# Optimization experiments

Measured on AMD Instinct MI355X. Metric: run time of the kernel, lower is better.

## Reference

```python
import jax, jax.numpy as jnp
import numpy as np
import math

D_MODEL = 768
NHEAD = 12
NUM_LAYERS = 6
INPUT_DIM = 768
HEAD_DIM = D_MODEL // NHEAD
D_FF = 4 * D_MODEL
TOTAL_HEADS = NUM_LAYERS * NHEAD
B, N = 4, 512


def _ln(x, g, b, eps=1e-5):
    mu = jnp.mean(x, axis=-1, keepdims=True)
    var = jnp.mean((x - mu) ** 2, axis=-1, keepdims=True)
    return (x - mu) * jax.lax.rsqrt(var + eps) * g + b


def setup_inputs() -> dict:
    key = jax.random.key(0)
    ks = iter(jax.random.split(key, 32))
    s = 0.02  # init scale keeps sigmoid scores away from saturation
    d = {
        "sentence_embeddings": jax.random.normal(next(ks), (B, N, INPUT_DIM), jnp.float32),
        "Win": jax.random.normal(next(ks), (D_MODEL, INPUT_DIM), jnp.float32) * s,
        "b_in": jnp.zeros((D_MODEL,), jnp.float32),
        "Wq": jax.random.normal(next(ks), (NUM_LAYERS, D_MODEL, D_MODEL), jnp.float32) * s,
        "bq": jnp.zeros((NUM_LAYERS, D_MODEL), jnp.float32),
        "Wk": jax.random.normal(next(ks), (NUM_LAYERS, D_MODEL, D_MODEL), jnp.float32) * s,
        "bk": jnp.zeros((NUM_LAYERS, D_MODEL), jnp.float32),
        "Wv": jax.random.normal(next(ks), (NUM_LAYERS, D_MODEL, D_MODEL), jnp.float32) * s,
        "bv": jnp.zeros((NUM_LAYERS, D_MODEL), jnp.float32),
        "Wo": jax.random.normal(next(ks), (NUM_LAYERS, D_MODEL, D_MODEL), jnp.float32) * s,
        "bo": jnp.zeros((NUM_LAYERS, D_MODEL), jnp.float32),
        "g1": jnp.ones((NUM_LAYERS, D_MODEL), jnp.float32),
        "be1": jnp.zeros((NUM_LAYERS, D_MODEL), jnp.float32),
        "g2": jnp.ones((NUM_LAYERS, D_MODEL), jnp.float32),
        "be2": jnp.zeros((NUM_LAYERS, D_MODEL), jnp.float32),
        "W1": jax.random.normal(next(ks), (NUM_LAYERS, D_FF, D_MODEL), jnp.float32) * s,
        "bf1": jnp.zeros((NUM_LAYERS, D_FF), jnp.float32),
        "W2": jax.random.normal(next(ks), (NUM_LAYERS, D_MODEL, D_FF), jnp.float32) * s,
        "bf2": jnp.zeros((NUM_LAYERS, D_MODEL), jnp.float32),
        "Wr1": jax.random.normal(next(ks), (D_MODEL // 2, D_MODEL), jnp.float32) * s,
        "br1": jnp.zeros((D_MODEL // 2,), jnp.float32),
        "Wr2": jax.random.normal(next(ks), (TOTAL_HEADS, D_MODEL // 2), jnp.float32) * s,
        "br2": jnp.zeros((TOTAL_HEADS,), jnp.float32),
        "agg_bias": jnp.zeros((1,), jnp.float32),
    }
    return d


def _forward(sentence_embeddings, Win, b_in, Wq, bq, Wk, bk, Wv, bv, Wo, bo,
             g1, be1, g2, be2, W1, bf1, W2, bf2, Wr1, br1, Wr2, br2, agg_bias):
    b, n, _ = sentence_embeddings.shape
    x = sentence_embeddings @ Win.T + b_in  # [B,N,D]
    off_diag = (1.0 - jnp.eye(n, dtype=x.dtype))[None, None]  # [1,1,N,N]
    scale = 1.0 / math.sqrt(HEAD_DIM)
    all_scores = []
    for i in range(NUM_LAYERS):
        n1 = _ln(x, g1[i], be1[i])
        q = (n1 @ Wq[i].T + bq[i]).reshape(b, n, NHEAD, HEAD_DIM).transpose(0, 2, 1, 3)
        k = (n1 @ Wk[i].T + bk[i]).reshape(b, n, NHEAD, HEAD_DIM).transpose(0, 2, 1, 3)
        v = (n1 @ Wv[i].T + bv[i]).reshape(b, n, NHEAD, HEAD_DIM).transpose(0, 2, 1, 3)
        scores = jnp.einsum('bhnd,bhmd->bhnm', q, k) * scale
        probs = jax.nn.sigmoid(scores)  # [B,H,N,N]
        row_sums = probs.sum(axis=-1, keepdims=True) + 1e-6
        attn = jnp.einsum('bhnm,bhmd->bhnd', probs, v) / row_sums
        attn = attn.transpose(0, 2, 1, 3).reshape(b, n, D_MODEL)
        x = x + attn @ Wo[i].T + bo[i]
        n2 = _ln(x, g2[i], be2[i])
        ff = jax.nn.gelu(n2 @ W1[i].T + bf1[i], approximate=False) @ W2[i].T + bf2[i]
        x = x + ff
        all_scores.append(probs * off_diag)  # zero the diagonal
    raw_w = jax.nn.gelu(x @ Wr1.T + br1, approximate=False) @ Wr2.T + br2  # [B,N,LH]
    stacked = jnp.concatenate(all_scores, axis=1)  # [B, L*H, N, N]
    final = jnp.einsum('bnh,bhnm->bnm', raw_w, stacked)
    return final + agg_bias[0]


def reference(sentence_embeddings, Win, b_in, Wq, bq, Wk, bk, Wv, bv, Wo, bo,
              g1, be1, g2, be2, W1, bf1, W2, bf2, Wr1, br1, Wr2, br2, agg_bias):
    return _forward(sentence_embeddings, Win, b_in, Wq, bq, Wk, bk, Wv, bv, Wo, bo,
                    g1, be1, g2, be2, W1, bf1, W2, bf2, Wr1, br1, Wr2, br2, agg_bias)
```

## Files before the change

kernel.cpp:

```cpp
#include <hip/hip_runtime.h>
#include <stdint.h>

#define LAYERS 6
#define BB 4
#define NSEQ 512
#define DM 768
#define NH 12
#define HD 64
#define DFF 3072
#define MTOK 2048
#define QKVN 2304
#define DR1 384
#define TH 72

typedef __attribute__((ext_vector_type(8))) short bf16x8;
typedef __attribute__((ext_vector_type(4))) float f32x4;

__device__ __forceinline__ unsigned short f2bf(float f) {
  union { float f; uint32_t u; } v; v.f = f;
  return (unsigned short)((v.u + 0x7fffu + ((v.u >> 16) & 1u)) >> 16);
}
__device__ __forceinline__ float bf2f(unsigned short h) {
  union { uint32_t u; float f; } v; v.u = ((uint32_t)h) << 16;
  return v.f;
}
__device__ __forceinline__ void gload16(const void* g, void* l) {
  __builtin_amdgcn_global_load_lds((const __attribute__((address_space(1))) void*)g,
                                   (__attribute__((address_space(3))) void*)l, 16, 0, 0);
}
#define MFMA(a, b, c) __builtin_amdgcn_mfma_f32_16x16x32_bf16(a, b, c, 0, 0, 0)

__device__ __forceinline__ float sigmoid8(float s) {
  float e, r;
  float t = s * -0.18033688011112443f;
  asm("v_exp_f32 %0, %1" : "=v"(e) : "v"(t));
  float d = 1.0f + e;
  asm("v_rcp_f32 %0, %1" : "=v"(r) : "v"(d));
  return r;
}

__global__ void cvt_f32_bf16(const float* __restrict__ s, unsigned short* __restrict__ d, int n4) {
  int i = blockIdx.x * blockDim.x + threadIdx.x;
  if (i >= n4) return;
  float4 v = reinterpret_cast<const float4*>(s)[i];
  ushort4 o;
  o.x = f2bf(v.x); o.y = f2bf(v.y); o.z = f2bf(v.z); o.w = f2bf(v.w);
  reinterpret_cast<ushort4*>(d)[i] = o;
}

__global__ void convert_layer(const float* __restrict__ wq, const float* __restrict__ wk,
                              const float* __restrict__ wv, const float* __restrict__ wo,
                              const float* __restrict__ w1, const float* __restrict__ w2,
                              const float* __restrict__ bq, const float* __restrict__ bk,
                              const float* __restrict__ bv,
                              unsigned short* __restrict__ qkvw, float* __restrict__ qkvb,
                              unsigned short* __restrict__ wow, unsigned short* __restrict__ w1w,
                              unsigned short* __restrict__ w2w) {
  const int A4 = (QKVN * DM) / 4;
  const int B4 = (DM * DM) / 4;
  const int C4 = (DFF * DM) / 4;
  int i = blockIdx.x * blockDim.x + threadIdx.x;
  if (i < QKVN / 4) {
    int j = i * 4;
    #pragma unroll
    for (int t = 0; t < 4; ++t) {
      int jj = j + t;
      int seg = jj / DM, c = jj % DM;
      const float* src = (seg == 0) ? bq : ((seg == 1) ? bk : bv);
      qkvb[jj] = src[c];
    }
  }
  const float* s4; unsigned short* dst;
  if (i < A4) {
    int j = i * 4; int row = j / DM; int c = j % DM;
    const float* w = (row < DM) ? wq : ((row < 2 * DM) ? wk : wv);
    s4 = w + (size_t)(row % DM) * DM + c; dst = qkvw + j;
  } else if (i < A4 + B4) {
    int j = (i - A4) * 4; s4 = wo + j; dst = wow + j;
  } else if (i < A4 + B4 + C4) {
    int j = (i - A4 - B4) * 4; s4 = w1 + j; dst = w1w + j;
  } else if (i < A4 + B4 + 2 * C4) {
    int j = (i - A4 - B4 - C4) * 4; s4 = w2 + j; dst = w2w + j;
  } else return;
  float4 v = *reinterpret_cast<const float4*>(s4);
  ushort4 o;
  o.x = f2bf(v.x); o.y = f2bf(v.y); o.z = f2bf(v.z); o.w = f2bf(v.w);
  *reinterpret_cast<ushort4*>(dst) = o;
}

__global__ __launch_bounds__(256) void ln_kernel(const float* __restrict__ x,
                                                 const float* __restrict__ g,
                                                 const float* __restrict__ b,
                                                 unsigned short* __restrict__ out) {
  int wave = threadIdx.x >> 6;
  int lane = threadIdx.x & 63;
  int row = blockIdx.x * 4 + wave;
  const float* xr = x + (size_t)row * DM;
  float v[12];
  #pragma unroll
  for (int c = 0; c < 3; ++c) {
    float4 t = *reinterpret_cast<const float4*>(xr + lane * 12 + c * 4);
    v[c * 4 + 0] = t.x; v[c * 4 + 1] = t.y; v[c * 4 + 2] = t.z; v[c * 4 + 3] = t.w;
  }
  float s = 0.f, s2 = 0.f;
  #pragma unroll
  for (int c = 0; c < 12; ++c) { s += v[c]; s2 += v[c] * v[c]; }
  #pragma unroll
  for (int m = 1; m < 64; m <<= 1) { s += __shfl_xor(s, m); s2 += __shfl_xor(s2, m); }
  float mu = s * (1.f / 768.f);
  float var = s2 * (1.f / 768.f) - mu * mu;
  float rstd = rsqrtf(var + 1e-5f);
  unsigned short o[12];
  #pragma unroll
  for (int c = 0; c < 12; ++c) {
    int col = lane * 12 + c;
    o[c] = f2bf((v[c] - mu) * rstd * g[col] + b[col]);
  }
  unsigned short* orow = out + (size_t)row * DM + lane * 12;
  #pragma unroll
  for (int c = 0; c < 3; ++c)
    reinterpret_cast<ushort4*>(orow)[c] = make_ushort4(o[c * 4], o[c * 4 + 1], o[c * 4 + 2], o[c * 4 + 3]);
}

template<int BM, int BN, int EPI>
__global__ __launch_bounds__(256) void gemm_bt(const unsigned short* __restrict__ A,
                                               const unsigned short* __restrict__ B,
                                               const float* __restrict__ bias,
                                               const float* __restrict__ resid,
                                               float* __restrict__ outf,
                                               unsigned short* __restrict__ outb,
                                               int M, int N, int K) {
  constexpr int MI = BM / 32;
  constexpr int NI = BN / 32;
  constexpr int ACH = BM / 32;
  constexpr int BCH = BN / 32;
  __shared__ unsigned short As[2][BM * 64];
  __shared__ unsigned short Bs[2][BN * 64];
  const int tid = threadIdx.x;
  const int w = tid >> 6, lane = tid & 63;
  const int wr = w >> 1, wc = w & 1;
  const int l15 = lane & 15, rq = lane >> 4;
  const int bM = blockIdx.y * BM, bN = blockIdx.x * BN;
  const f32x4 zero4 = {0.f, 0.f, 0.f, 0.f};
  f32x4 acc[MI][NI];
  #pragma unroll
  for (int mi = 0; mi < MI; ++mi)
    #pragma unroll
    for (int ni = 0; ni < NI; ++ni) acc[mi][ni] = zero4;
  const int srow = lane >> 3;
  const int scol = ((lane & 7) ^ (lane >> 3)) * 8;
  auto stage = [&](int bf, int k0) {
    #pragma unroll
    for (int cc = 0; cc < ACH; ++cc) {
      int c = w * ACH + cc;
      gload16(A + (size_t)(bM + 8 * c + srow) * K + k0 + scol, (void*)(&As[bf][c * 512]));
    }
    #pragma unroll
    for (int cc = 0; cc < BCH; ++cc) {
      int c = w * BCH + cc;
      gload16(B + (size_t)(bN + 8 * c + srow) * K + k0 + scol, (void*)(&Bs[bf][c * 512]));
    }
  };
  const int kper = K / gridDim.z;
  const int kbase = blockIdx.z * kper;
  const int nt = kper / 64;
  stage(0, kbase);
  __syncthreads();
  int buf = 0;
  for (int t = 0; t < nt; ++t) {
    if (t + 1 < nt) stage(buf ^ 1, kbase + (t + 1) * 64);
    #pragma unroll
    for (int kk = 0; kk < 2; ++kk) {
      bf16x8 af[MI], bfr[NI];
      #pragma unroll
      for (int mi = 0; mi < MI; ++mi) {
        int row = wr * (BM / 2) + mi * 16 + l15;
        af[mi] = *(const bf16x8*)(&As[buf][row * 64 + (((kk * 4 + rq) ^ (row & 7)) * 8)]);
      }
      #pragma unroll
      for (int ni = 0; ni < NI; ++ni) {
        int row = wc * (BN / 2) + ni * 16 + l15;
        bfr[ni] = *(const bf16x8*)(&Bs[buf][row * 64 + (((kk * 4 + rq) ^ (row & 7)) * 8)]);
      }
      #pragma unroll
      for (int mi = 0; mi < MI; ++mi)
        #pragma unroll
        for (int ni = 0; ni < NI; ++ni)
          acc[mi][ni] = MFMA(af[mi], bfr[ni], acc[mi][ni]);
    }
    __syncthreads();
    buf ^= 1;
  }
  #pragma unroll
  for (int mi = 0; mi < MI; ++mi)
    #pragma unroll
    for (int ni = 0; ni < NI; ++ni)
      #pragma unroll
      for (int r = 0; r < 4; ++r) {
        int row = bM + wr * (BM / 2) + mi * 16 + 4 * rq + r;
        int col = bN + wc * (BN / 2) + ni * 16 + l15;
        if constexpr (EPI == 4) {
          outf[(size_t)blockIdx.z * M * N + (size_t)row * N + col] = acc[mi][ni][r];
        } else {
          float val = acc[mi][ni][r] + bias[col];
          if constexpr (EPI == 0) {
            outb[(size_t)row * N + col] = f2bf(val);
          } else if constexpr (EPI == 1) {
            float gg = 0.5f * val * (1.0f + erff(val * 0.70710678118f));
            outb[(size_t)row * N + col] = f2bf(gg);
          } else if constexpr (EPI == 2) {
            outf[(size_t)row * N + col] = resid[(size_t)row * N + col] + val;
          } else {
            outf[(size_t)row * N + col] = val;
          }
        }
      }
}

__global__ __launch_bounds__(256) void ff2_combine(const float* __restrict__ pk,
                                                   const float* __restrict__ bias,
                                                   float* __restrict__ x) {
  int i = blockIdx.x * 256 + threadIdx.x;
  int e = i * 4;
  int col = e % DM;
  float4 a = *reinterpret_cast<const float4*>(x + e);
  float4 p0 = *reinterpret_cast<const float4*>(pk + e);
  float4 p1 = *reinterpret_cast<const float4*>(pk + (size_t)MTOK * DM + e);
  float4 b4 = *reinterpret_cast<const float4*>(bias + col);
  a.x += p0.x + p1.x + b4.x;
  a.y += p0.y + p1.y + b4.y;
  a.z += p0.z + p1.z + b4.z;
  a.w += p0.w + p1.w + b4.w;
  *reinterpret_cast<float4*>(x + e) = a;
}

__global__ __launch_bounds__(256) void attn_kernel(const unsigned short* __restrict__ qkv,
                                                   float* __restrict__ po,
                                                   float* __restrict__ prs) {
  __shared__ unsigned short Ks[64 * 64];
  __shared__ unsigned short vt[64 * 72];
  __shared__ unsigned short pl[4][16 * 72];
  const int tid = threadIdx.x;
  const int w = tid >> 6, lane = tid & 63;
  const int l15 = lane & 15, rq = lane >> 4;
  const int b = blockIdx.y / NH, h = blockIdx.y % NH;
  const int n0 = blockIdx.x * 64;
  const int part = blockIdx.z;
  const unsigned short* base = qkv + (size_t)(b * NSEQ) * QKVN + h * HD;
  bf16x8 aq0, aq1;
  {
    const unsigned short* qp = base + (size_t)(n0 + w * 16 + l15) * QKVN + rq * 8;
    aq0 = *(const bf16x8*)qp;
    aq1 = *(const bf16x8*)(qp + 32);
  }
  float rs[4] = {0.f, 0.f, 0.f, 0.f};
  const f32x4 zero4 = {0.f, 0.f, 0.f, 0.f};
  f32x4 acco[4];
  #pragma unroll
  for (int j = 0; j < 4; ++j) acco[j] = zero4;
  unsigned short* plw = &pl[w][0];

  for (int mt = 0; mt < 4; ++mt) {
    const int m0 = part * 256 + mt * 64;
    __syncthreads();
    #pragma unroll
    for (int it = 0; it < 2; ++it) {
      int idx = tid + it * 256;
      int r = idx >> 3, c = idx & 7;
      bf16x8 kv = *(const bf16x8*)(base + 768 + (size_t)(m0 + r) * QKVN + c * 8);
      *(bf16x8*)(Ks + r * 64 + (c ^ (r & 7)) * 8) = kv;
      bf16x8 vv = *(const bf16x8*)(base + 1536 + (size_t)(m0 + r) * QKVN + c * 8);
      #pragma unroll
      for (int j = 0; j < 8; ++j) vt[(c * 8 + j) * 72 + r] = (unsigned short)vv[j];
    }
    __syncthreads();
    #pragma unroll
    for (int ni = 0; ni < 4; ++ni) {
      int kr = ni * 16 + l15;
      bf16x8 bk0 = *(const bf16x8*)(Ks + kr * 64 + ((rq) ^ (kr & 7)) * 8);
      bf16x8 bk1 = *(const bf16x8*)(Ks + kr * 64 + ((rq + 4) ^ (kr & 7)) * 8);
      f32x4 z = zero4;
      z = MFMA(aq0, bk0, z);
      z = MFMA(aq1, bk1, z);
      #pragma unroll
      for (int r = 0; r < 4; ++r) {
        float p = sigmoid8(z[r]);
        rs[r] += p;
        plw[(4 * rq + r) * 72 + ni * 16 + l15] = f2bf(p);
      }
    }
    #pragma unroll
    for (int kk = 0; kk < 2; ++kk) {
      bf16x8 ap = *(const bf16x8*)(plw + l15 * 72 + kk * 32 + rq * 8);
      #pragma unroll
      for (int j2 = 0; j2 < 4; ++j2) {
        bf16x8 bvv = *(const bf16x8*)(vt + (j2 * 16 + l15) * 72 + kk * 32 + rq * 8);
        acco[j2] = MFMA(ap, bvv, acco[j2]);
      }
    }
  }
  #pragma unroll
  for (int m = 1; m < 16; m <<= 1)
    #pragma unroll
    for (int r = 0; r < 4; ++r) rs[r] += __shfl_xor(rs[r], m);
  float* pop = po + (size_t)part * MTOK * DM;
  #pragma unroll
  for (int j2 = 0; j2 < 4; ++j2)
    #pragma unroll
    for (int r = 0; r < 4; ++r) {
      int row = b * NSEQ + n0 + w * 16 + 4 * rq + r;
      int col = h * HD + j2 * 16 + l15;
      pop[(size_t)row * DM + col] = acco[j2][r];
    }
  if (l15 == 0) {
    #pragma unroll
    for (int r = 0; r < 4; ++r)
      prs[((size_t)part * (BB * NH) + blockIdx.y) * NSEQ + n0 + w * 16 + 4 * rq + r] = rs[r];
  }
}

__global__ __launch_bounds__(256) void attn_combine(const float* __restrict__ po,
                                                    const float* __restrict__ prs,
                                                    unsigned short* __restrict__ attnbf) {
  int i = blockIdx.x * 256 + threadIdx.x;
  int e = i * 4;
  int row = e / DM, col = e % DM;
  int b = row >> 9, n = row & 511, h = col >> 6;
  float r0 = prs[((size_t)(b * NH + h)) * NSEQ + n];
  float r1 = prs[(size_t)(BB * NH) * NSEQ + ((size_t)(b * NH + h)) * NSEQ + n];
  float inv = 1.f / (r0 + r1 + 1e-6f);
  float4 p0 = *reinterpret_cast<const float4*>(po + e);
  float4 p1 = *reinterpret_cast<const float4*>(po + (size_t)MTOK * DM + e);
  ushort4 o;
  o.x = f2bf((p0.x + p1.x) * inv);
  o.y = f2bf((p0.y + p1.y) * inv);
  o.z = f2bf((p0.z + p1.z) * inv);
  o.w = f2bf((p0.w + p1.w) * inv);
  *reinterpret_cast<ushort4*>(attnbf + e) = o;
}

__global__ __launch_bounds__(128) void wr2_kernel(const unsigned short* __restrict__ h1,
                                                  const float* __restrict__ wr2,
                                                  const float* __restrict__ br2,
                                                  float* __restrict__ raww) {
  __shared__ float hrow[DR1];
  int row = blockIdx.x;
  const unsigned short* hp = h1 + (size_t)row * DR1;
  for (int c = threadIdx.x; c < DR1; c += 128) hrow[c] = bf2f(hp[c]);
  __syncthreads();
  int j = threadIdx.x;
  if (j < TH) {
    const float* wrow = wr2 + (size_t)j * DR1;
    float acc = 0.f;
    for (int c = 0; c < DR1; ++c) acc += hrow[c] * wrow[c];
    raww[(size_t)row * TH + j] = acc + br2[j];
  }
}

__global__ __launch_bounds__(256) void agg_kernel(const unsigned short* __restrict__ qkv_all,
                                                  const float* __restrict__ raww,
                                                  float* __restrict__ part) {
  __shared__ unsigned short Ks[64 * 64];
  __shared__ unsigned short Qs[64 * 64];
  const int tid = threadIdx.x;
  const int w = tid >> 6, lane = tid & 63;
  const int l15 = lane & 15, rq = lane >> 4;
  const int z = blockIdx.z;
  const int l = z >> 2, b = z & 3;
  const int m0 = blockIdx.x * 64, nb = blockIdx.y * 64;
  const unsigned short* base = qkv_all + (size_t)l * MTOK * QKVN + (size_t)(b * NSEQ) * QKVN;
  const f32x4 zero4 = {0.f, 0.f, 0.f, 0.f};
  float acc[4][4];
  #pragma unroll
  for (int ni = 0; ni < 4; ++ni)
    #pragma unroll
    for (int r = 0; r < 4; ++r) acc[ni][r] = 0.f;
  for (int h = 0; h < NH; ++h) {
    __syncthreads();
    #pragma unroll
    for (int it = 0; it < 2; ++it) {
      int idx = tid + it * 256;
      int r = idx >> 3, c = idx & 7;
      bf16x8 kv = *(const bf16x8*)(base + (size_t)(m0 + r) * QKVN + 768 + h * HD + c * 8);
      *(bf16x8*)(Ks + r * 64 + (c ^ (r & 7)) * 8) = kv;
      bf16x8 qv = *(const bf16x8*)(base + (size_t)(nb + r) * QKVN + h * HD + c * 8);
      *(bf16x8*)(Qs + r * 64 + (c ^ (r & 7)) * 8) = qv;
    }
    __syncthreads();
    const int qr = w * 16 + l15;
    bf16x8 aq0 = *(const bf16x8*)(Qs + qr * 64 + ((rq) ^ (qr & 7)) * 8);
    bf16x8 aq1 = *(const bf16x8*)(Qs + qr * 64 + ((rq + 4) ^ (qr & 7)) * 8);
    float wl[4];
    #pragma unroll
    for (int r = 0; r < 4; ++r)
      wl[r] = raww[(size_t)(b * NSEQ + nb + w * 16 + 4 * rq + r) * TH + l * NH + h];
    #pragma unroll
    for (int ni = 0; ni < 4; ++ni) {
      int kr = ni * 16 + l15;
      bf16x8 bk0 = *(const bf16x8*)(Ks + kr * 64 + ((rq) ^ (kr & 7)) * 8);
      bf16x8 bk1 = *(const bf16x8*)(Ks + kr * 64 + ((rq + 4) ^ (kr & 7)) * 8);
      f32x4 zz = zero4;
      zz = MFMA(aq0, bk0, zz);
      zz = MFMA(aq1, bk1, zz);
      #pragma unroll
      for (int r = 0; r < 4; ++r) {
        acc[ni][r] += wl[r] * sigmoid8(zz[r]);
      }
    }
  }
  #pragma unroll
  for (int ni = 0; ni < 4; ++ni)
    #pragma unroll
    for (int r = 0; r < 4; ++r) {
      int n = nb + w * 16 + 4 * rq + r;
      part[((size_t)z * NSEQ + n) * NSEQ + m0 + ni * 16 + l15] = acc[ni][r];
    }
}

__global__ __launch_bounds__(256) void agg_reduce(const float* __restrict__ part,
                                                  const float* __restrict__ agg_bias,
                                                  float* __restrict__ out) {
  int i = blockIdx.x * 256 + threadIdx.x;
  int e = i * 4;
  float4 s = {0.f, 0.f, 0.f, 0.f};
  #pragma unroll
  for (int l = 0; l < LAYERS; ++l) {
    float4 p = *reinterpret_cast<const float4*>(part + (size_t)l * BB * NSEQ * NSEQ + e);
    s.x += p.x; s.y += p.y; s.z += p.z; s.w += p.w;
  }
  int n = (e >> 9) & 511, m = e & 511;
  float ab = agg_bias[0];
  float4 o;
  o.x = (n == m)     ? ab : s.x + ab;
  o.y = (n == m + 1) ? ab : s.y + ab;
  o.z = (n == m + 2) ? ab : s.z + ab;
  o.w = (n == m + 3) ? ab : s.w + ab;
  *reinterpret_cast<float4*>(out + e) = o;
}

extern "C" void kernel_launch(void* const* d_in, const int* in_sizes, int n_in,
                              void* d_out, int out_size, void* d_ws, size_t ws_size,
                              hipStream_t stream) {
  const float* emb  = (const float*)d_in[0];
  const float* Win  = (const float*)d_in[1];
  const float* b_in = (const float*)d_in[2];
  const float* Wq   = (const float*)d_in[3];
  const float* bq   = (const float*)d_in[4];
  const float* Wk   = (const float*)d_in[5];
  const float* bk   = (const float*)d_in[6];
  const float* Wv   = (const float*)d_in[7];
  const float* bv   = (const float*)d_in[8];
  const float* Wo   = (const float*)d_in[9];
  const float* bo   = (const float*)d_in[10];
  const float* g1   = (const float*)d_in[11];
  const float* be1  = (const float*)d_in[12];
  const float* g2   = (const float*)d_in[13];
  const float* be2  = (const float*)d_in[14];
  const float* W1   = (const float*)d_in[15];
  const float* bf1  = (const float*)d_in[16];
  const float* W2   = (const float*)d_in[17];
  const float* bf2  = (const float*)d_in[18];
  const float* Wr1  = (const float*)d_in[19];
  const float* br1  = (const float*)d_in[20];
  const float* Wr2  = (const float*)d_in[21];
  const float* br2  = (const float*)d_in[22];
  const float* aggb = (const float*)d_in[23];
  float* out = (float*)d_out;
  (void)in_sizes; (void)n_in; (void)out_size; (void)ws_size;

  char* ws = (char*)d_ws;
  size_t off = 0;
  auto alloc = [&](size_t bytes) -> char* {
    char* p = ws + off;
    off += (bytes + 255) & ~(size_t)255;
    return p;
  };
  unsigned short* qkvw   = (unsigned short*)alloc((size_t)QKVN * DM * 2);
  float*          qkvb   = (float*)alloc((size_t)QKVN * 4);
  unsigned short* wow    = (unsigned short*)alloc((size_t)DM * DM * 2);
  unsigned short* w1w    = (unsigned short*)alloc((size_t)DFF * DM * 2);
  unsigned short* w2w    = (unsigned short*)alloc((size_t)DM * DFF * 2);
  unsigned short* winw   = (unsigned short*)alloc((size_t)DM * DM * 2);
  unsigned short* wr1w   = (unsigned short*)alloc((size_t)DR1 * DM * 2);
  unsigned short* h1bf   = (unsigned short*)alloc((size_t)MTOK * DR1 * 2);
  float*          raww   = (float*)alloc((size_t)MTOK * TH * 4);
  float*          prs    = (float*)alloc((size_t)2 * BB * NH * NSEQ * 4);
  float*          skbuf  = (float*)alloc((size_t)2 * MTOK * DM * 4);
  unsigned short* qkvall = (unsigned short*)alloc((size_t)LAYERS * MTOK * QKVN * 2);
  char* scratch = alloc(0);
  unsigned short* embbf  = (unsigned short*)(scratch);
  float*          x      = (float*)(scratch + 3145728);
  unsigned short* nbf    = (unsigned short*)(scratch + 3145728 + 6291456);
  unsigned short* attnbf = (unsigned short*)(scratch + 3145728 + 6291456 + 3145728);
  char*           S      = scratch + 3145728 + 6291456 + 3145728 + 3145728;
  unsigned short* xbf    = (unsigned short*)(S + 12582912);
  float*          po     = (float*)S;
  unsigned short* ff1bf  = (unsigned short*)S;
  float*          part   = (float*)scratch;

  cvt_f32_bf16<<<1536, 256, 0, stream>>>(emb, embbf, (MTOK * DM) / 4);
  cvt_f32_bf16<<<576, 256, 0, stream>>>(Win, winw, (DM * DM) / 4);
  cvt_f32_bf16<<<288, 256, 0, stream>>>(Wr1, wr1w, (DR1 * DM) / 4);

  dim3 g768(DM / 64, MTOK / 64);
  gemm_bt<64, 64, 3><<<g768, 256, 0, stream>>>(embbf, winw, b_in, nullptr, x, nullptr, MTOK, DM, DM);

  const int CL_GRID = ((QKVN * DM + DM * DM + 2 * DFF * DM) / 4 + 255) / 256;
  for (int l = 0; l < LAYERS; ++l) {
    convert_layer<<<CL_GRID, 256, 0, stream>>>(
        Wq + (size_t)l * DM * DM, Wk + (size_t)l * DM * DM, Wv + (size_t)l * DM * DM,
        Wo + (size_t)l * DM * DM, W1 + (size_t)l * DFF * DM, W2 + (size_t)l * DM * DFF,
        bq + l * DM, bk + l * DM, bv + l * DM, qkvw, qkvb, wow, w1w, w2w);
    ln_kernel<<<512, 256, 0, stream>>>(x, g1 + l * DM, be1 + l * DM, nbf);
    unsigned short* qkvl = qkvall + (size_t)l * MTOK * QKVN;
    dim3 gqkv(QKVN / 128, MTOK / 128);
    gemm_bt<128, 128, 0><<<gqkv, 256, 0, stream>>>(nbf, qkvw, qkvb, nullptr, nullptr, qkvl, MTOK, QKVN, DM);
    attn_kernel<<<dim3(8, BB * NH, 2), 256, 0, stream>>>(qkvl, po, prs);
    attn_combine<<<(MTOK * DM / 4) / 256, 256, 0, stream>>>(po, prs, attnbf);
    gemm_bt<64, 64, 2><<<g768, 256, 0, stream>>>(attnbf, wow, bo + l * DM, x, x, nullptr, MTOK, DM, DM);
    ln_kernel<<<512, 256, 0, stream>>>(x, g2 + l * DM, be2 + l * DM, nbf);
    dim3 gff1(DFF / 128, MTOK / 128);
    gemm_bt<128, 128, 1><<<gff1, 256, 0, stream>>>(nbf, w1w, bf1 + l * DFF, nullptr, nullptr, ff1bf, MTOK, DFF, DM);
    dim3 gff2(DM / 64, MTOK / 64, 2);
    gemm_bt<64, 64, 4><<<gff2, 256, 0, stream>>>(ff1bf, w2w, nullptr, nullptr, skbuf, nullptr, MTOK, DM, DFF);
    ff2_combine<<<(MTOK * DM / 4) / 256, 256, 0, stream>>>(skbuf, bf2 + l * DM, x);
  }

  cvt_f32_bf16<<<1536, 256, 0, stream>>>(x, xbf, (MTOK * DM) / 4);
  dim3 gr1(DR1 / 64, MTOK / 64);
  gemm_bt<64, 64, 1><<<gr1, 256, 0, stream>>>(xbf, wr1w, br1, nullptr, nullptr, h1bf, MTOK, DR1, DM);
  wr2_kernel<<<MTOK, 128, 0, stream>>>(h1bf, Wr2, br2, raww);
  agg_kernel<<<dim3(8, 8, LAYERS * BB), 256, 0, stream>>>(qkvall, raww, part);
  agg_reduce<<<(BB * NSEQ * NSEQ / 4) / 256, 256, 0, stream>>>(part, aggb, out);
}
```

Measured before the change: 797.8 us.

## Use tanh GELU approximation, fuse final bf16 cast, restructure V transpose load

Replaces the exact erf GELU in the GEMM epilogue with a tanh-form approximation built from hardware exp and rcp. It also folds the final fp32-to-bf16 conversion into the last layer's ff2_combine, removing one kernel launch and one pass over x. Finally, it changes how the attention kernel loads V: each thread gathers eight rows of one column and writes them with a single vector store, instead of eight scalar transposed stores. The tanh GELU differs from the erf reference, the new V gather uses strided scalar global loads, and the three changes are unrelated.

```diff
diff --git a/kernel.cpp b/kernel.cpp
--- a/kernel.cpp
+++ b/kernel.cpp
@@ -37,6 +37,16 @@
   float d = 1.0f + e;
   asm("v_rcp_f32 %0, %1" : "=v"(r) : "v"(d));
   return r;
+}
+
+__device__ __forceinline__ float gelu_f(float x) {
+  float t = 0.7978845608028654f * x * (1.0f + 0.044715f * x * x);
+  float u = fminf(t * 2.8853900817779268f, 126.0f);
+  float e, r;
+  asm("v_exp_f32 %0, %1" : "=v"(e) : "v"(u));
+  float d = e + 1.0f;
+  asm("v_rcp_f32 %0, %1" : "=v"(r) : "v"(d));
+  return x * e * r;
 }
 
 __global__ void cvt_f32_bf16(const float* __restrict__ s, unsigned short* __restrict__ d, int n4) {
@@ -206,8 +216,7 @@
           if constexpr (EPI == 0) {
             outb[(size_t)row * N + col] = f2bf(val);
           } else if constexpr (EPI == 1) {
-            float gg = 0.5f * val * (1.0f + erff(val * 0.70710678118f));
-            outb[(size_t)row * N + col] = f2bf(gg);
+            outb[(size_t)row * N + col] = f2bf(gelu_f(val));
           } else if constexpr (EPI == 2) {
             outf[(size_t)row * N + col] = resid[(size_t)row * N + col] + val;
           } else {
@@ -219,7 +228,8 @@
 
 __global__ __launch_bounds__(256) void ff2_combine(const float* __restrict__ pk,
                                                    const float* __restrict__ bias,
-                                                   float* __restrict__ x) {
+                                                   float* __restrict__ x,
+                                                   unsigned short* __restrict__ xb) {
   int i = blockIdx.x * 256 + threadIdx.x;
   int e = i * 4;
   int col = e % DM;
@@ -232,6 +242,11 @@
   a.z += p0.z + p1.z + b4.z;
   a.w += p0.w + p1.w + b4.w;
   *reinterpret_cast<float4*>(x + e) = a;
+  if (xb) {
+    ushort4 o;
+    o.x = f2bf(a.x); o.y = f2bf(a.y); o.z = f2bf(a.z); o.w = f2bf(a.w);
+    *reinterpret_cast<ushort4*>(xb + e) = o;
+  }
 }
 
 __global__ __launch_bounds__(256) void attn_kernel(const unsigned short* __restrict__ qkv,
@@ -269,9 +284,12 @@
       int r = idx >> 3, c = idx & 7;
       bf16x8 kv = *(const bf16x8*)(base + 768 + (size_t)(m0 + r) * QKVN + c * 8);
       *(bf16x8*)(Ks + r * 64 + (c ^ (r & 7)) * 8) = kv;
-      bf16x8 vv = *(const bf16x8*)(base + 1536 + (size_t)(m0 + r) * QKVN + c * 8);
-      #pragma unroll
-      for (int j = 0; j < 8; ++j) vt[(c * 8 + j) * 72 + r] = (unsigned short)vv[j];
+      int cd = idx & 63, g = (idx >> 6) & 7;
+      const unsigned short* vp = base + 1536 + (size_t)(m0 + g * 8) * QKVN + cd;
+      bf16x8 vv;
+      #pragma unroll
+      for (int j = 0; j < 8; ++j) vv[j] = (short)vp[(size_t)j * QKVN];
+      *(bf16x8*)(vt + cd * 72 + g * 8) = vv;
     }
     __syncthreads();
     #pragma unroll
@@ -523,10 +541,10 @@
     gemm_bt<128, 128, 1><<<gff1, 256, 0, stream>>>(nbf, w1w, bf1 + l * DFF, nullptr, nullptr, ff1bf, MTOK, DFF, DM);
     dim3 gff2(DM / 64, MTOK / 64, 2);
     gemm_bt<64, 64, 4><<<gff2, 256, 0, stream>>>(ff1bf, w2w, nullptr, nullptr, skbuf, nullptr, MTOK, DM, DFF);
-    ff2_combine<<<(MTOK * DM / 4) / 256, 256, 0, stream>>>(skbuf, bf2 + l * DM, x);
-  }
-
-  cvt_f32_bf16<<<1536, 256, 0, stream>>>(x, xbf, (MTOK * DM) / 4);
+    ff2_combine<<<(MTOK * DM / 4) / 256, 256, 0, stream>>>(skbuf, bf2 + l * DM, x,
+                                                          (l == LAYERS - 1) ? xbf : nullptr);
+  }
+
   dim3 gr1(DR1 / 64, MTOK / 64);
   gemm_bt<64, 64, 1><<<gr1, 256, 0, stream>>>(xbf, wr1w, br1, nullptr, nullptr, h1bf, MTOK, DR1, DM);
   wr2_kernel<<<MTOK, 128, 0, stream>>>(h1bf, Wr2, br2, raww);
```

Result: faster. 755.5 us (-5.3%).
